# Performance work log

Hardware: AMD Instinct MI355X
Metric: run time of the kernel (lower is better)

The kernel has to match this reference:

```python
import jax, jax.numpy as jnp
import numpy as np

# NF4 codebook (bitsandbytes nf4 data type, 16 levels)
NF4_TABLE = np.array([
    -1.0, -0.6961928009986877, -0.5250730514526367, -0.39491748809814453,
    -0.28444138169288635, -0.18477343022823334, -0.09105003625154495, 0.0,
    0.07958029955625534, 0.16093020141124725, 0.24611230194568634,
    0.33791524171829224, 0.44070982933044434, 0.5626170039176941,
    0.7229568362236023, 1.0], dtype=np.float32)

BLOCKSIZE = 64
SCALING = 32.0 / 16.0  # lora_alpha / r


def setup_inputs() -> dict:
    key = jax.random.key(0)
    k1, k2, k3, k4, k5 = jax.random.split(key, 5)
    tokens, in_f, out_f, r = 256, 4096, 11008, 16
    x = jax.random.normal(k1, (tokens, in_f), dtype=jnp.float32)
    q_codes = jax.random.randint(k2, (out_f, in_f), 0, 16, dtype=jnp.int32)
    absmax = jax.random.uniform(k3, (out_f, in_f // BLOCKSIZE), dtype=jnp.float32)
    lora_A = jax.random.normal(k4, (r, in_f), dtype=jnp.float32) * (1.0 / np.sqrt(in_f))
    lora_B = jax.random.normal(k5, (out_f, r), dtype=jnp.float32) * 0.02
    return {"x": x, "q_codes": q_codes, "absmax": absmax,
            "lora_A": lora_A, "lora_B": lora_B}


def reference(x, q_codes, absmax, lora_A, lora_B):
    out_f, in_f = q_codes.shape
    nf4 = jnp.asarray(NF4_TABLE, dtype=x.dtype)
    # Dequantize: codebook lookup, then per-block absmax scale.
    W = nf4[q_codes].reshape(out_f, in_f // BLOCKSIZE, BLOCKSIZE)
    W = (W * absmax[:, :, None]).reshape(out_f, in_f)  # [out_f, in_f]
    # Base 4-bit linear (no bias in bnb Linear4bit default here).
    base = x @ W.T  # [tokens, out_f]
    # LoRA path: dropout p=0 is identity in eval; scaling = alpha/r.
    lora = (x @ lora_A.T) @ lora_B.T  # [tokens, r] -> [tokens, out_f]
    return base + lora * jnp.asarray(SCALING, dtype=x.dtype)
```

## Files before the change

### kernel.cpp

```cpp
#include <hip/hip_runtime.h>
#include <hip/hip_fp16.h>

typedef unsigned int uint;
typedef unsigned short ushort;

typedef __attribute__((ext_vector_type(8))) _Float16 f16x8;
typedef __attribute__((ext_vector_type(4))) float f32x4;

#define TOK 256
#define OUTF 11008
#define INF 4096
#define BM 256
#define BN 64
#define NT2 172

__device__ __constant__ float NF4_TBL[16] = {
    -1.0f, -0.6961928009986877f, -0.5250730514526367f, -0.39491748809814453f,
    -0.28444138169288635f, -0.18477343022823334f, -0.09105003625154495f, 0.0f,
    0.07958029955625534f, 0.16093020141124725f, 0.24611230194568634f,
    0.33791524171829224f, 0.44070982933044434f, 0.5626170039176941f,
    0.7229568362236023f, 1.0f};

__device__ __forceinline__ ushort f2h(float f) {
  return __half_as_ushort(__float2half(f));
}

__device__ __forceinline__ void async_cp16(const void* g, void* l) {
  __builtin_amdgcn_global_load_lds(
      (const __attribute__((address_space(1))) uint*)g,
      (__attribute__((address_space(3))) uint*)l, 16, 0, 0);
}

__device__ __forceinline__ float nf4v(int c, int tbits) {
  return __int_as_float(__builtin_amdgcn_ds_bpermute(c << 2, tbits));
}

__device__ __forceinline__ uint2 dq4(int4 c, __half2 ax2, int tbits) {
  __half2 h0 = __floats2half2_rn(nf4v(c.x, tbits), nf4v(c.y, tbits));
  __half2 h1 = __floats2half2_rn(nf4v(c.z, tbits), nf4v(c.w, tbits));
  h0 = __hmul2(h0, ax2);
  h1 = __hmul2(h1, ax2);
  union { __half2 h[2]; uint2 u; } r;
  r.h[0] = h0; r.h[1] = h1;
  return r.u;
}

__global__ void prep_kernel(const float4* __restrict__ x4, ushort4* __restrict__ xh4,
                            const float4* __restrict__ lB4, ushort4* __restrict__ lBh4) {
  const int stride = gridDim.x * blockDim.x;
  const int t0 = blockIdx.x * blockDim.x + threadIdx.x;
  for (int i = t0; i < TOK * INF / 4; i += stride) {
    float4 v = x4[i];
    ushort4 o;
    o.x = f2h(v.x); o.y = f2h(v.y); o.z = f2h(v.z); o.w = f2h(v.w);
    xh4[i] = o;
  }
  for (int i = t0; i < OUTF * 16; i += stride) {
    int n = i >> 4, jq = i & 15;
    ushort4 o = {0, 0, 0, 0};
    if (jq < 4) {
      float4 v = lB4[n * 4 + jq];
      o.x = f2h(v.x); o.y = f2h(v.y); o.z = f2h(v.z); o.w = f2h(v.w);
    }
    lBh4[i] = o;
  }
}

__global__ __launch_bounds__(1024)
void xa_kernel(const float* __restrict__ x, const float* __restrict__ lA,
               ushort* __restrict__ xa2) {
  const int m = blockIdx.x;
  const int t = threadIdx.x;
  const float4* x4 = (const float4*)(x + (size_t)m * INF);
  const float4* lA4 = (const float4*)lA;
  float4 xv = x4[t];
  float acc[16];
#pragma unroll
  for (int j = 0; j < 16; ++j) {
    float4 a = lA4[j * (INF / 4) + t];
    acc[j] = xv.x * a.x + xv.y * a.y + xv.z * a.z + xv.w * a.w;
  }
#pragma unroll
  for (int j = 0; j < 16; ++j)
#pragma unroll
    for (int s = 32; s > 0; s >>= 1) acc[j] += __shfl_xor(acc[j], s, 64);
  __shared__ float red[16][16];
  const int w = t >> 6, l = t & 63;
  if (l == 0) {
#pragma unroll
    for (int j = 0; j < 16; ++j) red[w][j] = acc[j];
  }
  __syncthreads();
  if (t < 64) {
    ushort v = 0;
    if (t < 16) {
      float s = 0.f;
#pragma unroll
      for (int w2 = 0; w2 < 16; ++w2) s += red[w2][t];
      v = f2h(2.0f * s);
    }
    xa2[m * 64 + t] = v;
  }
}

__global__ __launch_bounds__(256, 3)
void gemm_kernel(const int* __restrict__ qc, const float* __restrict__ am,
                 const ushort* __restrict__ xh, const ushort* __restrict__ lBh,
                 const ushort* __restrict__ xa2, float* __restrict__ dest, int nst) {
  __shared__ ushort Abuf[BM * 64];
  __shared__ ushort Bbuf[64 * 64];
  __shared__ float Qax[1024];

  const int tid = threadIdx.x;
  const int w = tid >> 6;
  const int l = tid & 63;
  const int chunk = l >> 4;
  const int rlo = l & 15;
  const int split = blockIdx.x / NT2;
  const int ntile = blockIdx.x - split * NT2;
  const int n0 = ntile * BN;
  const int kb0 = split * nst;

  const int tbits = __float_as_int(NF4_TBL[l & 15]);

  const int arow = w * 8 + (l >> 3);
  const int acol = ((l & 7) ^ (l >> 3)) << 3;
  int aoff[2][4];
#pragma unroll
  for (int ks2 = 0; ks2 < 2; ++ks2) {
    const int cc = ks2 * 4 + chunk;
#pragma unroll
    for (int mt = 0; mt < 4; ++mt)
      aoff[ks2][mt] = (w * 64 + mt * 16 + rlo) * 64 + ((cc ^ (l & 7)) << 3);
  }

  const int qrg = tid >> 4;
  const int qch = tid & 15;
  const int* qbase[4];
  int bdst[4];
#pragma unroll
  for (int p = 0; p < 4; ++p) {
    int r = p * 16 + qrg;
    qbase[p] = qc + (size_t)(n0 + r) * INF + kb0 * 64 + qch * 4;
    bdst[p] = r * 64 + (((qch >> 1) ^ (r & 7)) << 3) + (qch & 1) * 4;
  }

  int boff[2][4];
#pragma unroll
  for (int ks2 = 0; ks2 < 2; ++ks2)
#pragma unroll
    for (int nt = 0; nt < 4; ++nt)
      boff[ks2][nt] = (nt * 16 + rlo) * 64 + (((ks2 * 4 + chunk) ^ (rlo & 7)) << 3);

  f32x4 acc[4][4];
#pragma unroll
  for (int mt = 0; mt < 4; ++mt)
#pragma unroll
    for (int nt = 0; nt < 4; ++nt) acc[mt][nt] = (f32x4){0.f, 0.f, 0.f, 0.f};

  if (w == 0) {
#pragma unroll
    for (int j = 0; j < 4; ++j)
      async_cp16(am + (size_t)(n0 + l) * 64 + kb0 + j * 4, (char*)Qax + j * 1024);
  }
#pragma unroll
  for (int i = 0; i < 8; ++i) {
    const ushort* g = xh + (size_t)(i * 32 + arow) * INF + kb0 * 64 + acol;
    async_cp16(g, &Abuf[(i * 256 + w * 64) * 8]);
  }
  int4 qreg[4];
#pragma unroll
  for (int p = 0; p < 4; ++p) qreg[p] = *(const int4*)(qbase[p]);

  for (int s = 0; s < nst; ++s) {
    __syncthreads();

    const int sl = s & 15;
#pragma unroll
    for (int p = 0; p < 4; ++p) {
      int r = p * 16 + qrg;
      __half2 ax2 = __float2half2_rn(Qax[(sl >> 2) * 256 + r * 4 + (sl & 3)]);
      *(uint2*)&Bbuf[bdst[p]] = dq4(qreg[p], ax2, tbits);
    }
    f16x8 areg[2][4];
#pragma unroll
    for (int ks2 = 0; ks2 < 2; ++ks2)
#pragma unroll
      for (int mt = 0; mt < 4; ++mt) areg[ks2][mt] = *(const f16x8*)&Abuf[aoff[ks2][mt]];

    __syncthreads();

    if (s + 1 < nst) {
      const int kb = kb0 + s + 1;
#pragma unroll
      for (int i = 0; i < 8; ++i) {
        const ushort* g = xh + (size_t)(i * 32 + arow) * INF + kb * 64 + acol;
        async_cp16(g, &Abuf[(i * 256 + w * 64) * 8]);
      }
#pragma unroll
      for (int p = 0; p < 4; ++p) qreg[p] = *(const int4*)(qbase[p] + (s + 1) * 64);
      if (((s + 1) & 15) == 0 && w == 0) {
#pragma unroll
        for (int j = 0; j < 4; ++j)
          async_cp16(am + (size_t)(n0 + l) * 64 + kb0 + s + 1 + j * 4, (char*)Qax + j * 1024);
      }
    }

#pragma unroll
    for (int ks2 = 0; ks2 < 2; ++ks2) {
      f16x8 b[4];
#pragma unroll
      for (int nt = 0; nt < 4; ++nt) b[nt] = *(const f16x8*)&Bbuf[boff[ks2][nt]];
#pragma unroll
      for (int mt = 0; mt < 4; ++mt)
#pragma unroll
        for (int nt = 0; nt < 4; ++nt)
          acc[mt][nt] = __builtin_amdgcn_mfma_f32_16x16x32_f16(areg[ks2][mt], b[nt], acc[mt][nt], 0, 0, 0);
    }
  }

  if (split == 0) {
    f16x8 a_l[4], b_l[4];
#pragma unroll
    for (int mt = 0; mt < 4; ++mt)
      a_l[mt] = *(const f16x8*)(xa2 + (size_t)(w * 64 + mt * 16 + rlo) * 64 + chunk * 8);
#pragma unroll
    for (int nt = 0; nt < 4; ++nt)
      b_l[nt] = *(const f16x8*)(lBh + (size_t)(n0 + nt * 16 + rlo) * 64 + chunk * 8);
#pragma unroll
    for (int mt = 0; mt < 4; ++mt)
#pragma unroll
      for (int nt = 0; nt < 4; ++nt)
        acc[mt][nt] = __builtin_amdgcn_mfma_f32_16x16x32_f16(a_l[mt], b_l[nt], acc[mt][nt], 0, 0, 0);
  }

  float* dst = dest + (size_t)split * TOK * OUTF;
#pragma unroll
  for (int mt = 0; mt < 4; ++mt) {
#pragma unroll
    for (int nt = 0; nt < 4; ++nt) {
      int c = n0 + nt * 16 + rlo;
#pragma unroll
      for (int r = 0; r < 4; ++r) {
        int row = w * 64 + mt * 16 + chunk * 4 + r;
        dst[(size_t)row * OUTF + c] = acc[mt][nt][r];
      }
    }
  }
}

__global__ void reduce_kernel(const float4* __restrict__ part, float4* __restrict__ out,
                              int ks) {
  const int QN = TOK * OUTF / 4;
  int i = blockIdx.x * blockDim.x + threadIdx.x;
  if (i < QN) {
    float4 s = part[i];
    for (int s2 = 1; s2 < ks; ++s2) {
      float4 p = part[(size_t)s2 * QN + i];
      s.x += p.x; s.y += p.y; s.z += p.z; s.w += p.w;
    }
    out[i] = s;
  }
}

extern "C" void kernel_launch(void* const* d_in, const int* in_sizes, int n_in,
                              void* d_out, int out_size, void* d_ws, size_t ws_size,
                              hipStream_t stream) {
  const float* x = (const float*)d_in[0];
  const int* qc = (const int*)d_in[1];
  const float* am = (const float*)d_in[2];
  const float* lA = (const float*)d_in[3];
  const float* lB = (const float*)d_in[4];
  float* out = (float*)d_out;

  const size_t off_lB = (size_t)TOK * INF * 2;
  const size_t off_xa2 = off_lB + (size_t)OUTF * 64 * 2;
  const size_t off_part = off_xa2 + (size_t)TOK * 64 * 2;
  const size_t part_bytes = (size_t)TOK * OUTF * 4;

  ushort* xh = (ushort*)d_ws;
  ushort* lBh = (ushort*)((char*)d_ws + off_lB);
  ushort* xa2 = (ushort*)((char*)d_ws + off_xa2);
  float* part = (float*)((char*)d_ws + off_part);

  int ks = 1;
  if (ws_size >= off_part + 4 * part_bytes) ks = 4;
  else if (ws_size >= off_part + 2 * part_bytes) ks = 2;
  float* dest = (ks == 1) ? out : part;

  prep_kernel<<<2048, 256, 0, stream>>>((const float4*)x, (ushort4*)xh,
                                        (const float4*)lB, (ushort4*)lBh);
  xa_kernel<<<TOK, 1024, 0, stream>>>(x, lA, xa2);
  gemm_kernel<<<NT2 * ks, 256, 0, stream>>>(qc, am, xh, lBh, xa2, dest, 64 / ks);
  if (ks > 1)
    reduce_kernel<<<(TOK * OUTF / 4 + 255) / 256, 256, 0, stream>>>((const float4*)part,
                                                                    (float4*)out, ks);
}
```

Baseline: 309.4 us.

## Use atomic split-K accumulation, fuse prep kernels, double-buffer NF4 code prefetch

The split-K GEMM now always uses four splits and adds its partial tiles straight into the output with unsafeAtomicAdd. This removes the partial-sum workspace and the separate reduce kernel. The FP16 conversion and the x·Aᵀ LoRA projection are merged into one launch, which also zeroes the output beforehand. The quantized-code registers are double-buffered, so the next step's codes are loaded at the top of the loop before the dequantize. The trade is atomic contention on the output, an extra output zeroing pass, and summation order that is no longer deterministic.

```diff
diff --git a/kernel.cpp b/kernel.cpp
--- a/kernel.cpp
+++ b/kernel.cpp
@@ -13,6 +13,8 @@
 #define BM 256
 #define BN 64
 #define NT2 172
+#define CVT_BLKS 2048
+#define KSPLIT 4
 
 __device__ __constant__ float NF4_TBL[16] = {
     -1.0f, -0.6961928009986877f, -0.5250730514526367f, -0.39491748809814453f,
@@ -45,68 +47,75 @@
   return r.u;
 }
 
-__global__ void prep_kernel(const float4* __restrict__ x4, ushort4* __restrict__ xh4,
-                            const float4* __restrict__ lB4, ushort4* __restrict__ lBh4) {
-  const int stride = gridDim.x * blockDim.x;
-  const int t0 = blockIdx.x * blockDim.x + threadIdx.x;
-  for (int i = t0; i < TOK * INF / 4; i += stride) {
-    float4 v = x4[i];
-    ushort4 o;
-    o.x = f2h(v.x); o.y = f2h(v.y); o.z = f2h(v.z); o.w = f2h(v.w);
-    xh4[i] = o;
-  }
-  for (int i = t0; i < OUTF * 16; i += stride) {
-    int n = i >> 4, jq = i & 15;
-    ushort4 o = {0, 0, 0, 0};
-    if (jq < 4) {
-      float4 v = lB4[n * 4 + jq];
+__global__ __launch_bounds__(256)
+void prep_kernel(const float4* __restrict__ x4, ushort4* __restrict__ xh4,
+                 const float4* __restrict__ lB4, ushort4* __restrict__ lBh4,
+                 const float* __restrict__ x, const float* __restrict__ lA,
+                 ushort* __restrict__ xa2, float4* __restrict__ out4) {
+  if (blockIdx.x < CVT_BLKS) {
+    const int stride = CVT_BLKS * blockDim.x;
+    const int t0 = blockIdx.x * blockDim.x + threadIdx.x;
+    for (int i = t0; i < TOK * INF / 4; i += stride) {
+      float4 v = x4[i];
+      ushort4 o;
       o.x = f2h(v.x); o.y = f2h(v.y); o.z = f2h(v.z); o.w = f2h(v.w);
-    }
-    lBh4[i] = o;
-  }
-}
-
-__global__ __launch_bounds__(1024)
-void xa_kernel(const float* __restrict__ x, const float* __restrict__ lA,
-               ushort* __restrict__ xa2) {
-  const int m = blockIdx.x;
-  const int t = threadIdx.x;
-  const float4* x4 = (const float4*)(x + (size_t)m * INF);
-  const float4* lA4 = (const float4*)lA;
-  float4 xv = x4[t];
-  float acc[16];
-#pragma unroll
-  for (int j = 0; j < 16; ++j) {
-    float4 a = lA4[j * (INF / 4) + t];
-    acc[j] = xv.x * a.x + xv.y * a.y + xv.z * a.z + xv.w * a.w;
-  }
-#pragma unroll
-  for (int j = 0; j < 16; ++j)
-#pragma unroll
-    for (int s = 32; s > 0; s >>= 1) acc[j] += __shfl_xor(acc[j], s, 64);
-  __shared__ float red[16][16];
-  const int w = t >> 6, l = t & 63;
-  if (l == 0) {
-#pragma unroll
-    for (int j = 0; j < 16; ++j) red[w][j] = acc[j];
-  }
-  __syncthreads();
-  if (t < 64) {
-    ushort v = 0;
-    if (t < 16) {
-      float s = 0.f;
-#pragma unroll
-      for (int w2 = 0; w2 < 16; ++w2) s += red[w2][t];
-      v = f2h(2.0f * s);
-    }
-    xa2[m * 64 + t] = v;
+      xh4[i] = o;
+    }
+    for (int i = t0; i < OUTF * 16; i += stride) {
+      int n = i >> 4, jq = i & 15;
+      ushort4 o = {0, 0, 0, 0};
+      if (jq < 4) {
+        float4 v = lB4[n * 4 + jq];
+        o.x = f2h(v.x); o.y = f2h(v.y); o.z = f2h(v.z); o.w = f2h(v.w);
+      }
+      lBh4[i] = o;
+    }
+    const float4 z = {0.f, 0.f, 0.f, 0.f};
+    for (int i = t0; i < TOK * OUTF / 4; i += stride) out4[i] = z;
+  } else {
+    const int m = blockIdx.x - CVT_BLKS;
+    const int t = threadIdx.x;
+    const float4* xm4 = (const float4*)(x + (size_t)m * INF);
+    const float4* lA4 = (const float4*)lA;
+    float4 xv[4];
+#pragma unroll
+    for (int c = 0; c < 4; ++c) xv[c] = xm4[c * 256 + t];
+    float acc[16];
+#pragma unroll
+    for (int j = 0; j < 16; ++j) {
+      acc[j] = 0.f;
+#pragma unroll
+      for (int c = 0; c < 4; ++c) {
+        float4 a = lA4[j * (INF / 4) + c * 256 + t];
+        acc[j] += xv[c].x * a.x + xv[c].y * a.y + xv[c].z * a.z + xv[c].w * a.w;
+      }
+    }
+#pragma unroll
+    for (int j = 0; j < 16; ++j)
+#pragma unroll
+      for (int s = 32; s > 0; s >>= 1) acc[j] += __shfl_xor(acc[j], s, 64);
+    __shared__ float red[4][16];
+    const int w = t >> 6, l = t & 63;
+    if (l == 0) {
+#pragma unroll
+      for (int j = 0; j < 16; ++j) red[w][j] = acc[j];
+    }
+    __syncthreads();
+    if (t < 64) {
+      ushort v = 0;
+      if (t < 16) {
+        float s = red[0][t] + red[1][t] + red[2][t] + red[3][t];
+        v = f2h(2.0f * s);
+      }
+      xa2[m * 64 + t] = v;
+    }
   }
 }
 
 __global__ __launch_bounds__(256, 3)
 void gemm_kernel(const int* __restrict__ qc, const float* __restrict__ am,
                  const ushort* __restrict__ xh, const ushort* __restrict__ lBh,
-                 const ushort* __restrict__ xa2, float* __restrict__ dest, int nst) {
+                 const ushort* __restrict__ xa2, float* __restrict__ out, int nst) {
   __shared__ ushort Abuf[BM * 64];
   __shared__ ushort Bbuf[64 * 64];
   __shared__ float Qax[1024];
@@ -168,19 +177,26 @@
     const ushort* g = xh + (size_t)(i * 32 + arow) * INF + kb0 * 64 + acol;
     async_cp16(g, &Abuf[(i * 256 + w * 64) * 8]);
   }
-  int4 qreg[4];
-#pragma unroll
-  for (int p = 0; p < 4; ++p) qreg[p] = *(const int4*)(qbase[p]);
+  int4 qreg[2][4];
+#pragma unroll
+  for (int p = 0; p < 4; ++p) qreg[0][p] = *(const int4*)(qbase[p]);
 
   for (int s = 0; s < nst; ++s) {
+    const int par = s & 1;
     __syncthreads();
+
+    if (s + 1 < nst) {
+#pragma unroll
+      for (int p = 0; p < 4; ++p)
+        qreg[par ^ 1][p] = *(const int4*)(qbase[p] + (s + 1) * 64);
+    }
 
     const int sl = s & 15;
 #pragma unroll
     for (int p = 0; p < 4; ++p) {
       int r = p * 16 + qrg;
       __half2 ax2 = __float2half2_rn(Qax[(sl >> 2) * 256 + r * 4 + (sl & 3)]);
-      *(uint2*)&Bbuf[bdst[p]] = dq4(qreg[p], ax2, tbits);
+      *(uint2*)&Bbuf[bdst[p]] = dq4(qreg[par][p], ax2, tbits);
     }
     f16x8 areg[2][4];
 #pragma unroll
@@ -197,13 +213,6 @@
         const ushort* g = xh + (size_t)(i * 32 + arow) * INF + kb * 64 + acol;
         async_cp16(g, &Abuf[(i * 256 + w * 64) * 8]);
       }
-#pragma unroll
-      for (int p = 0; p < 4; ++p) qreg[p] = *(const int4*)(qbase[p] + (s + 1) * 64);
-      if (((s + 1) & 15) == 0 && w == 0) {
-#pragma unroll
-        for (int j = 0; j < 4; ++j)
-          async_cp16(am + (size_t)(n0 + l) * 64 + kb0 + s + 1 + j * 4, (char*)Qax + j * 1024);
-      }
     }
 
 #pragma unroll
@@ -234,7 +243,6 @@
         acc[mt][nt] = __builtin_amdgcn_mfma_f32_16x16x32_f16(a_l[mt], b_l[nt], acc[mt][nt], 0, 0, 0);
   }
 
-  float* dst = dest + (size_t)split * TOK * OUTF;
 #pragma unroll
   for (int mt = 0; mt < 4; ++mt) {
 #pragma unroll
@@ -243,23 +251,9 @@
 #pragma unroll
       for (int r = 0; r < 4; ++r) {
         int row = w * 64 + mt * 16 + chunk * 4 + r;
-        dst[(size_t)row * OUTF + c] = acc[mt][nt][r];
-      }
-    }
-  }
-}
-
-__global__ void reduce_kernel(const float4* __restrict__ part, float4* __restrict__ out,
-                              int ks) {
-  const int QN = TOK * OUTF / 4;
-  int i = blockIdx.x * blockDim.x + threadIdx.x;
-  if (i < QN) {
-    float4 s = part[i];
-    for (int s2 = 1; s2 < ks; ++s2) {
-      float4 p = part[(size_t)s2 * QN + i];
-      s.x += p.x; s.y += p.y; s.z += p.z; s.w += p.w;
-    }
-    out[i] = s;
+        unsafeAtomicAdd(&out[(size_t)row * OUTF + c], acc[mt][nt][r]);
+      }
+    }
   }
 }
 
@@ -275,24 +269,12 @@
 
   const size_t off_lB = (size_t)TOK * INF * 2;
   const size_t off_xa2 = off_lB + (size_t)OUTF * 64 * 2;
-  const size_t off_part = off_xa2 + (size_t)TOK * 64 * 2;
-  const size_t part_bytes = (size_t)TOK * OUTF * 4;
-
   ushort* xh = (ushort*)d_ws;
   ushort* lBh = (ushort*)((char*)d_ws + off_lB);
   ushort* xa2 = (ushort*)((char*)d_ws + off_xa2);
-  float* part = (float*)((char*)d_ws + off_part);
-
-  int ks = 1;
-  if (ws_size >= off_part + 4 * part_bytes) ks = 4;
-  else if (ws_size >= off_part + 2 * part_bytes) ks = 2;
-  float* dest = (ks == 1) ? out : part;
-
-  prep_kernel<<<2048, 256, 0, stream>>>((const float4*)x, (ushort4*)xh,
-                                        (const float4*)lB, (ushort4*)lBh);
-  xa_kernel<<<TOK, 1024, 0, stream>>>(x, lA, xa2);
-  gemm_kernel<<<NT2 * ks, 256, 0, stream>>>(qc, am, xh, lBh, xa2, dest, 64 / ks);
-  if (ks > 1)
-    reduce_kernel<<<(TOK * OUTF / 4 + 255) / 256, 256, 0, stream>>>((const float4*)part,
-                                                                    (float4*)out, ks);
-}
+
+  prep_kernel<<<CVT_BLKS + TOK, 256, 0, stream>>>(
+      (const float4*)x, (ushort4*)xh, (const float4*)lB, (ushort4*)lBh,
+      x, lA, xa2, (float4*)out);
+  gemm_kernel<<<NT2 * KSPLIT, 256, 0, stream>>>(qc, am, xh, lBh, xa2, out, 64 / KSPLIT);
+}
```

Measured after the change: 349.5 us. 1.13x slower.
